# Performance work log

Measured on AMD Instinct MI355X. Metric: run time of the kernel, lower is better.

## Reference

```python
import jax, jax.numpy as jnp
import numpy as np

N = 100000      # nodes
E = 1000000     # edges
D_IN = 64       # in_channels
HID = 64        # hid_channels
ENC = 64        # encoding_dim
OUT = 2         # out_channels (classes)
EDGE_DIM = 32   # TimeEncode dim == edge_dim
HEADS = 2
HD = HID // 2   # per-head channels (32)


def _p(k, shape):
    s = 1.0 / np.sqrt(shape[0])
    return jax.random.uniform(k, shape, jnp.float32, -s, s)


def setup_inputs() -> dict:
    key = jax.random.key(0)
    ks = jax.random.split(key, 40)
    inp = {
        "x": jax.random.normal(ks[0], (N, D_IN), jnp.float32),
        "edge_index": jax.random.randint(ks[1], (2, E), 0, N),
        "node_time": jax.random.uniform(ks[2], (N,), jnp.float32) * 100.0,
        "edge_time": jax.random.uniform(ks[3], (E, 1), jnp.float32) * 100.0,
        "node_mean_out_time_interval": jax.random.uniform(ks[4], (N,), jnp.float32) * 10.0,
        "node_out_degree": jax.random.uniform(ks[5], (N,), jnp.float32) * 50.0,
        "y": jax.random.randint(ks[6], (N,), 0, OUT),
        "train_mask": jnp.ones((N,), bool),
        # TimeEncode: cos(t W + b)
        "time_w": _p(ks[7], (1, EDGE_DIM)), "time_b": jnp.zeros((EDGE_DIM,), jnp.float32),
        # TemporalFrequencyEncoder / DegreeEncoder: Linear(1, ENC)
        "tf_w": _p(ks[8], (1, ENC)), "tf_b": jnp.zeros((ENC,), jnp.float32),
        "deg_w": _p(ks[9], (1, ENC)), "deg_b": jnp.zeros((ENC,), jnp.float32),
        # lin: Linear(in, hid)
        "lin_w": _p(ks[10], (D_IN, HID)), "lin_b": jnp.zeros((HID,), jnp.float32),
        # TransformerConv projections (heads*HD = HID)
        "Wq": _p(ks[11], (HID, HEADS * HD)), "bq": jnp.zeros((HEADS * HD,), jnp.float32),
        "Wk": _p(ks[12], (HID, HEADS * HD)), "bk": jnp.zeros((HEADS * HD,), jnp.float32),
        "Wv": _p(ks[13], (HID, HEADS * HD)), "bv": jnp.zeros((HEADS * HD,), jnp.float32),
        "We": _p(ks[14], (EDGE_DIM, HEADS * HD)), "be": jnp.zeros((HEADS * HD,), jnp.float32),
        "Wskip": _p(ks[15], (HID, HEADS * HD)), "bskip": jnp.zeros((HEADS * HD,), jnp.float32),
        # size-2 context attention
        "wenc_w": _p(ks[16], (ENC, ENC)), "wenc_b": jnp.zeros((ENC,), jnp.float32),
        "wx_w": _p(ks[17], (HID, ENC)), "wx_b": jnp.zeros((ENC,), jnp.float32),
        # lin_combine: Linear(hid+enc, hid)
        "comb_w": _p(ks[18], (HID + ENC, HID)), "comb_b": jnp.zeros((HID,), jnp.float32),
        # out: Linear(hid, out)
        "out_w": _p(ks[19], (HID, OUT)), "out_b": jnp.zeros((OUT,), jnp.float32),
    }
    return inp


def reference(x, edge_index, node_time, edge_time, node_mean_out_time_interval,
              node_out_degree, y, train_mask,
              time_w, time_b, tf_w, tf_b, deg_w, deg_b, lin_w, lin_b,
              Wq, bq, Wk, bk, Wv, bv, We, be, Wskip, bskip,
              wenc_w, wenc_b, wx_w, wx_b, comb_w, comb_b, out_w, out_b):
    src, dst = edge_index[0], edge_index[1]

    # relative edge time -> TimeEncode (cos features), used as edge_attr [E, 32]
    rel_t = node_time[src][:, None] - edge_time          # [E,1]
    rel_t_enc = jnp.cos(rel_t @ time_w + time_b)         # [E,EDGE_DIM]

    h = jax.nn.relu(x @ lin_w + lin_b)                   # [N,HID] (dropout = identity, eval)

    # TransformerConv (PyG math): per-edge attention + scatter-softmax aggregate
    q = (h @ Wq + bq).reshape(N, HEADS, HD)[dst]          # [E,H,HD]
    e = (rel_t_enc @ We + be).reshape(E, HEADS, HD)       # [E,H,HD]
    k = (h @ Wk + bk).reshape(N, HEADS, HD)[src] + e
    v = (h @ Wv + bv).reshape(N, HEADS, HD)[src] + e
    alpha = (q * k).sum(-1) / np.float32(np.sqrt(HD))     # [E,H]
    m = jax.ops.segment_max(alpha, dst, num_segments=N)   # stable softmax per dst node
    ea = jnp.exp(alpha - m[dst])
    denom = jax.ops.segment_sum(ea, dst, num_segments=N)
    a = ea / (denom[dst] + 1e-16)
    agg = jax.ops.segment_sum(a[:, :, None] * v, dst, num_segments=N)
    h1 = agg.reshape(N, HEADS * HD) + h @ Wskip + bskip   # concat heads + root skip

    # size-2 context attention over (temporal-frequency, degree) encodings
    tf_enc = node_mean_out_time_interval[:, None] @ tf_w + tf_b   # [N,ENC]
    deg_enc = node_out_degree[:, None] @ deg_w + deg_b            # [N,ENC]
    enc = jnp.stack((tf_enc, deg_enc), axis=1)                    # [N,2,ENC]
    enc_proj = jnp.tanh(enc @ wenc_w + wenc_b)                    # [N,2,ENC]
    x_proj = jnp.tanh(h1 @ wx_w + wx_b)                           # [N,ENC]
    score = jax.nn.softmax(jnp.einsum('nkd,nd->nk', enc_proj, x_proj), axis=1)  # [N,2]
    context = enc[:, 0] * score[:, 0:1] + enc[:, 1] * score[:, 1:2]

    h1 = jnp.concatenate((h1, context), axis=1) @ comb_w + comb_b  # [N,HID]
    logp = jax.nn.log_softmax(h1 @ out_w + out_b, axis=1)          # [N,OUT]
    return (h1, logp, y, train_mask)
```

## Files before the change

kernel.cpp:

```cpp
#include <hip/hip_runtime.h>
#include <hip/hip_fp16.h>

#define DEV __device__ __forceinline__

typedef _Float16 f16x8 __attribute__((ext_vector_type(8)));
typedef float f32x4 __attribute__((ext_vector_type(4)));

DEV float mask_val(const unsigned char* mb, int n) {
  unsigned b0 = mb[0], b1 = mb[1], b2 = mb[2], b3 = mb[3];
  if (b0 <= 1u && b1 == b0 && b2 == b0 && b3 == b0) {
    return mb[n] ? 1.f : 0.f;
  } else if (b1 == 0u && b2 == 0u && b3 == 0u) {
    return ((const int*)mb)[n] ? 1.f : 0.f;
  } else {
    return (((const float*)mb)[n] != 0.f) ? 1.f : 0.f;
  }
}

DEV float head_sum32(float x) {
  x += __int_as_float(__builtin_amdgcn_ds_swizzle(__float_as_int(x), 0x041F));
  x += __int_as_float(__builtin_amdgcn_ds_swizzle(__float_as_int(x), 0x081F));
  x += __int_as_float(__builtin_amdgcn_ds_swizzle(__float_as_int(x), 0x101F));
  x += __int_as_float(__builtin_amdgcn_ds_swizzle(__float_as_int(x), 0x201F));
  x += __int_as_float(__builtin_amdgcn_ds_swizzle(__float_as_int(x), 0x401F));
  return x;
}

__global__ __launch_bounds__(256) void k_setup(
    const float* __restrict__ tf_w, const float* __restrict__ tf_b,
    const float* __restrict__ deg_w, const float* __restrict__ deg_b,
    const float* __restrict__ wenc_w, const float* __restrict__ wenc_b,
    const float* __restrict__ comb_w,
    const float* __restrict__ lin_w, const float* __restrict__ Wq,
    const float* __restrict__ Wk, const float* __restrict__ Wv,
    const float* __restrict__ Wsk,
    float* __restrict__ cbuf, _Float16* __restrict__ wt,
    int* __restrict__ counts, int N) {
  const int bid = blockIdx.x;
  if (bid < 80) {
    const float* Ws[5] = {lin_w, Wq, Wk, Wv, Wsk};
    int idx = bid * 256 + threadIdx.x;
    if (idx < 5 * 4096) {
      int s = idx >> 12, r = idx & 4095;
      int j = r >> 6, c = r & 63;
      wt[(s << 12) + c * 64 + j] = (_Float16)Ws[s][j * 64 + c];
    }
  } else if (bid == 80) {
    if (threadIdx.x < 64) {
      int c = threadIdx.x;
      float A0 = 0, B0 = 0, A1 = 0, B1 = 0, P0 = 0, Q0 = 0, P1 = 0, Q1 = 0;
      for (int j = 0; j < 64; ++j) {
        float w  = wenc_w[j * 64 + c];
        float cw = comb_w[(64 + j) * 64 + c];
        float twj = tf_w[j], tbj = tf_b[j], dwj = deg_w[j], dbj = deg_b[j];
        A0 += twj * w;  B0 += tbj * w;
        A1 += dwj * w;  B1 += dbj * w;
        P0 += twj * cw; Q0 += tbj * cw;
        P1 += dwj * cw; Q1 += dbj * cw;
      }
      float wb = wenc_b[c];
      cbuf[c]       = A0; cbuf[64 + c]  = B0 + wb;
      cbuf[128 + c] = A1; cbuf[192 + c] = B1 + wb;
      cbuf[256 + c] = P0; cbuf[320 + c] = Q0;
      cbuf[384 + c] = P1; cbuf[448 + c] = Q1;
    }
  } else {
    const int i = (bid - 81) * 256 + threadIdx.x;
    if (i < N) counts[i] = 0;
  }
}

__global__ __launch_bounds__(256) void k_node_proj(
    const float* __restrict__ x, const _Float16* __restrict__ wt,
    const float* __restrict__ lin_b, const float* __restrict__ bq,
    const float* __restrict__ bk, const float* __restrict__ bv,
    const float* __restrict__ bsk, const float* __restrict__ be,
    float* __restrict__ q, __half2* __restrict__ kvp,
    float* __restrict__ skipout, int N,
    const int* __restrict__ ei, int* __restrict__ counts,
    int* __restrict__ rank, int E, int ntiles) {
  __shared__ _Float16 H[4][16 * 72];
  const int bid = blockIdx.x;
  const int tid = threadIdx.x;
  if (bid >= ntiles) {
    const int i = (bid - ntiles) * 256 + tid;
    if (i < E) rank[i] = atomicAdd(&counts[ei[E + i]], 1);
    return;
  }
  const int lane = tid & 63;
  const int wv = tid >> 6;
  const int mrow = lane & 15;
  const int kgrp = lane >> 4;
  const float invs = 0.17677669529663687f;
  float b_lin[4], b_q[4], b_k[4], b_v[4], b_sk[4];
#pragma unroll
  for (int nt = 0; nt < 4; ++nt) {
    const int cc = nt * 16 + mrow;
    b_lin[nt] = lin_b[cc];
    b_q[nt] = bq[cc];
    b_k[nt] = bk[cc] + be[cc];
    b_v[nt] = bv[cc] + be[cc];
    b_sk[nt] = bsk[cc];
  }
  _Float16* Hw = H[wv];
  const int base = bid << 6;
  const int rowA = base + wv * 16 + mrow;
  const int rclamp = (rowA < N) ? rowA : (N - 1);
  const float* xr = x + (size_t)rclamp * 64 + kgrp * 8;
  const float4 u0 = *(const float4*)xr;
  const float4 u1 = *(const float4*)(xr + 4);
  const float4 u2 = *(const float4*)(xr + 32);
  const float4 u3 = *(const float4*)(xr + 36);
  const f16x8 a0 = {(_Float16)u0.x, (_Float16)u0.y, (_Float16)u0.z, (_Float16)u0.w,
                    (_Float16)u1.x, (_Float16)u1.y, (_Float16)u1.z, (_Float16)u1.w};
  const f16x8 a1 = {(_Float16)u2.x, (_Float16)u2.y, (_Float16)u2.z, (_Float16)u2.w,
                    (_Float16)u3.x, (_Float16)u3.y, (_Float16)u3.z, (_Float16)u3.w};
#pragma unroll
  for (int nt = 0; nt < 4; ++nt) {
    const _Float16* wb0 = wt + (nt * 16 + mrow) * 64 + kgrp * 8;
    const f16x8 B0 = *(const f16x8*)wb0;
    const f16x8 B1 = *(const f16x8*)(wb0 + 32);
    f32x4 C = {0.f, 0.f, 0.f, 0.f};
    C = __builtin_amdgcn_mfma_f32_16x16x32_f16(a0, B0, C, 0, 0, 0);
    C = __builtin_amdgcn_mfma_f32_16x16x32_f16(a1, B1, C, 0, 0, 0);
#pragma unroll
    for (int r = 0; r < 4; ++r) {
      const float hval = fmaxf(C[r] + b_lin[nt], 0.f);
      Hw[(kgrp * 4 + r) * 72 + nt * 16 + mrow] = (_Float16)hval;
    }
  }
  const f16x8 ha0 = *(const f16x8*)(Hw + mrow * 72 + kgrp * 8);
  const f16x8 ha1 = *(const f16x8*)(Hw + mrow * 72 + 32 + kgrp * 8);
  const int orow0 = base + wv * 16 + kgrp * 4;
#pragma unroll
  for (int nt = 0; nt < 4; ++nt) {
    const _Float16* wb0 = wt + 4096 + (nt * 16 + mrow) * 64 + kgrp * 8;
    const f16x8 B0 = *(const f16x8*)wb0;
    const f16x8 B1 = *(const f16x8*)(wb0 + 32);
    f32x4 C = {0.f, 0.f, 0.f, 0.f};
    C = __builtin_amdgcn_mfma_f32_16x16x32_f16(ha0, B0, C, 0, 0, 0);
    C = __builtin_amdgcn_mfma_f32_16x16x32_f16(ha1, B1, C, 0, 0, 0);
#pragma unroll
    for (int r = 0; r < 4; ++r) {
      const int orow = orow0 + r;
      if (orow < N) q[(size_t)orow * 64 + nt * 16 + mrow] = (C[r] + b_q[nt]) * invs;
    }
  }
#pragma unroll
  for (int nt = 0; nt < 4; ++nt) {
    const _Float16* wk0 = wt + 2 * 4096 + (nt * 16 + mrow) * 64 + kgrp * 8;
    const _Float16* wv0 = wt + 3 * 4096 + (nt * 16 + mrow) * 64 + kgrp * 8;
    const f16x8 Bk0 = *(const f16x8*)wk0;
    const f16x8 Bk1 = *(const f16x8*)(wk0 + 32);
    const f16x8 Bv0 = *(const f16x8*)wv0;
    const f16x8 Bv1 = *(const f16x8*)(wv0 + 32);
    f32x4 Ck = {0.f, 0.f, 0.f, 0.f};
    f32x4 Cv = {0.f, 0.f, 0.f, 0.f};
    Ck = __builtin_amdgcn_mfma_f32_16x16x32_f16(ha0, Bk0, Ck, 0, 0, 0);
    Ck = __builtin_amdgcn_mfma_f32_16x16x32_f16(ha1, Bk1, Ck, 0, 0, 0);
    Cv = __builtin_amdgcn_mfma_f32_16x16x32_f16(ha0, Bv0, Cv, 0, 0, 0);
    Cv = __builtin_amdgcn_mfma_f32_16x16x32_f16(ha1, Bv1, Cv, 0, 0, 0);
#pragma unroll
    for (int r = 0; r < 4; ++r) {
      const int orow = orow0 + r;
      if (orow < N)
        kvp[(size_t)orow * 64 + nt * 16 + mrow] =
            __halves2half2(__float2half_rn(Ck[r] + b_k[nt]), __float2half_rn(Cv[r] + b_v[nt]));
    }
  }
#pragma unroll
  for (int nt = 0; nt < 4; ++nt) {
    const _Float16* wb0 = wt + 4 * 4096 + (nt * 16 + mrow) * 64 + kgrp * 8;
    const f16x8 B0 = *(const f16x8*)wb0;
    const f16x8 B1 = *(const f16x8*)(wb0 + 32);
    f32x4 C = {0.f, 0.f, 0.f, 0.f};
    C = __builtin_amdgcn_mfma_f32_16x16x32_f16(ha0, B0, C, 0, 0, 0);
    C = __builtin_amdgcn_mfma_f32_16x16x32_f16(ha1, B1, C, 0, 0, 0);
#pragma unroll
    for (int r = 0; r < 4; ++r) {
      const int orow = orow0 + r;
      if (orow < N) skipout[(size_t)orow * 64 + nt * 16 + mrow] = C[r] + b_sk[nt];
    }
  }
}

__global__ __launch_bounds__(256) void k_scan1(const int* __restrict__ counts, int* __restrict__ excl,
                                               int* __restrict__ bsum, int N) {
  __shared__ int s[256];
  const int t = threadIdx.x;
  const int idx = blockIdx.x * 256 + t;
  int val = (idx < N) ? counts[idx] : 0;
  s[t] = val;
  __syncthreads();
  for (int d = 1; d < 256; d <<= 1) {
    int add = (t >= d) ? s[t - d] : 0;
    __syncthreads();
    s[t] += add;
    __syncthreads();
  }
  if (idx < N) excl[idx] = s[t] - val;
  if (t == 255) bsum[blockIdx.x] = s[255];
}

__global__ __launch_bounds__(1024) void k_scan2(int* __restrict__ bsum, int B) {
  __shared__ int sm[1024];
  const int t = threadIdx.x;
  if (B <= 1024) {
    int val = (t < B) ? bsum[t] : 0;
    sm[t] = val;
    __syncthreads();
    for (int d = 1; d < 1024; d <<= 1) {
      int add = (t >= d) ? sm[t - d] : 0;
      __syncthreads();
      sm[t] += add;
      __syncthreads();
    }
    if (t < B) bsum[t] = sm[t] - val;
  } else if (t == 0) {
    int acc = 0;
    for (int i = 0; i < B; ++i) { int tt = bsum[i]; bsum[i] = acc; acc += tt; }
  }
}

__global__ __launch_bounds__(256) void k_scan3(const int* __restrict__ bsum, int* __restrict__ rowptr,
                                               int N, int E) {
  int i = blockIdx.x * 256 + threadIdx.x;
  if (i < N) rowptr[i] = rowptr[i] + bsum[i >> 8];
  if (i == 0) rowptr[N] = E;
}

__global__ __launch_bounds__(256) void k_fill(const int* __restrict__ ei,
                                              const float* __restrict__ node_time,
                                              const float* __restrict__ edge_time,
                                              const int* __restrict__ rowptr,
                                              const int* __restrict__ rank,
                                              int2* __restrict__ er, int E) {
  int e = blockIdx.x * 256 + threadIdx.x;
  if (e < E) {
    int s = ei[e], d = ei[E + e];
    int pos = rowptr[d] + rank[e];
    er[pos] = make_int2(s, __float_as_int(node_time[s] - edge_time[e]));
  }
}

__global__ __launch_bounds__(256) void k_aggregate(
    const int* __restrict__ rowptr, const int2* __restrict__ er,
    const float* __restrict__ q, const unsigned* __restrict__ kvu,
    const float* __restrict__ time_w, const float* __restrict__ time_b,
    const float* __restrict__ We,
    float* __restrict__ h1, int N) {
  __shared__ float swS[4][64];
  __shared__ float EAs[4][2][16];
  const int tid = threadIdx.x;
  const int c = tid & 63;
  const int wv = tid >> 6;
  const float INV2PI = 0.15915494309189535f;
  float wcol[32], Gw[32];
#pragma unroll
  for (int j = 0; j < 32; ++j) wcol[j] = We[j * 64 + c];
#pragma unroll
  for (int j = 0; j < 32; ++j) Gw[j] = We[(c & 31) * 64 + (c & 32) + j];
  const float tw = time_w[c & 31] * INV2PI;
  const float tb = time_b[c & 31] * INV2PI;
  const int h32 = c & 32;
  const int lc = c & 15;
  const bool writer = (c & 16) == 0;
  float (*eaF)[16] = EAs[wv];
  const int n0 = blockIdx.x * 4 + wv;
  const int nstride = gridDim.x * 4;
  for (int n = n0; n < N; n += nstride) {
    const int start = __builtin_amdgcn_readfirstlane(rowptr[n]);
    const int end = __builtin_amdgcn_readfirstlane(rowptr[n + 1]);
    const float skipv = h1[(size_t)n * 64 + c];
    const float qc = q[(size_t)n * 64 + c];
    swS[wv][c] = qc;
    float Gc = 0.f;
#pragma unroll
    for (int j = 0; j < 32; ++j) Gc = fmaf(swS[wv][h32 | j], Gw[j], Gc);
    float m = -1e30f, den = 0.f, num = 0.f, S = 0.f;
    for (int ce = start; ce < end; ce += 16) {
      const int cnt = (end - ce < 16) ? (end - ce) : 16;
      int src_[16];
      float rr_[16];
#pragma unroll
      for (int i = 0; i < 16; ++i) {
        const int ee = ce + ((i < cnt) ? i : cnt - 1);
        const int2 a = er[ee];
        src_[i] = a.x;
        rr_[i] = __int_as_float(a.y);
      }
      unsigned kvr[16];
#pragma unroll
      for (int i = 0; i < 16; ++i) kvr[i] = kvu[(unsigned)(src_[i] * 64 + c)];
      float rv_[16], p[16];
#pragma unroll
      for (int i = 0; i < 16; ++i) {
        float ang = fmaf(rr_[i], tw, tb);
        ang = ang - floorf(ang);
        rv_[i] = __builtin_amdgcn_cosf(ang);
        const __half2 h2 = *(const __half2*)&kvr[i];
        p[i] = fmaf(rv_[i], Gc, qc * __half2float(h2.x));
      }
#pragma unroll
      for (int i = 0; i < 16; ++i) p[i] = head_sum32(p[i]);
#pragma unroll
      for (int i = 0; i < 16; ++i)
        if (i >= cnt) p[i] = -1e30f;
      float cm = p[0];
#pragma unroll
      for (int i = 1; i < 16; ++i) cm = fmaxf(cm, p[i]);
      const float mn = fmaxf(m, cm);
      const float sc = __expf(m - mn);
      num *= sc; den *= sc; S *= sc; m = mn;
      if (writer) {
        float pv = p[0];
#pragma unroll
        for (int i = 1; i < 16; ++i) pv = (lc == i) ? p[i] : pv;
        eaF[c >> 5][lc] = __expf(pv - m);
      }
      const float* eah = eaF[h32 ? 1 : 0];
      const float4 e0 = ((const float4*)eah)[0];
      const float4 e1 = ((const float4*)eah)[1];
      const float4 e2 = ((const float4*)eah)[2];
      const float4 e3 = ((const float4*)eah)[3];
      const float ea_[16] = {e0.x, e0.y, e0.z, e0.w, e1.x, e1.y, e1.z, e1.w,
                             e2.x, e2.y, e2.z, e2.w, e3.x, e3.y, e3.z, e3.w};
#pragma unroll
      for (int i = 0; i < 16; ++i) {
        const float eai = ea_[i];
        const __half2 h2 = *(const __half2*)&kvr[i];
        num = fmaf(eai, __half2float(h2.y), num);
        S = fmaf(eai, rv_[i], S);
        den += eai;
      }
    }
    swS[wv][c] = S;
    float econ = 0.f;
#pragma unroll
    for (int j = 0; j < 32; ++j) econ = fmaf(swS[wv][h32 | j], wcol[j], econ);
    const float agg = (num + econ) / (den + 1e-16f);
    h1[(size_t)n * 64 + c] = agg + skipv;
  }
}

__global__ __launch_bounds__(256) void k_epilogue(
    const float* __restrict__ t_int, const float* __restrict__ deg,
    const float* __restrict__ cbuf,
    const float* __restrict__ wx_w, const float* __restrict__ wx_b,
    const float* __restrict__ comb_w, const float* __restrict__ comb_b,
    const float* __restrict__ out_w, const float* __restrict__ out_b,
    const int* __restrict__ y, const unsigned char* __restrict__ maskb,
    float* __restrict__ out, int N) {
  __shared__ float sh[4][64];
  const int tid = threadIdx.x;
  const int c = tid & 63;
  const int wv = tid >> 6;
  float wxreg[64], cbreg[64];
#pragma unroll
  for (int j = 0; j < 64; ++j) { wxreg[j] = wx_w[j * 64 + c]; cbreg[j] = comb_w[j * 64 + c]; }
  const float A0 = cbuf[c], B0 = cbuf[64 + c], A1 = cbuf[128 + c], B1 = cbuf[192 + c];
  const float P0 = cbuf[256 + c], Q0 = cbuf[320 + c], P1 = cbuf[384 + c], Q1 = cbuf[448 + c];
  const float wxb = wx_b[c], cbb = comb_b[c];
  const float ow0 = out_w[c * 2 + 0], ow1 = out_w[c * 2 + 1];
  const float ob0 = out_b[0], ob1 = out_b[1];
  const size_t O1 = (size_t)N * 64;
  const size_t O2 = O1 + (size_t)N * 2;
  const size_t O3 = O2 + (size_t)N;
  const int ngroups = (N + 3) >> 2;
  for (int g = blockIdx.x; g < ngroups; g += gridDim.x) {
    const int n = g * 4 + wv;
    const bool act = n < N;
    float h1a = 0.f, ti = 0.f, dg = 0.f;
    if (act) {
      h1a = out[(size_t)n * 64 + c];
      ti = t_int[n];
      dg = deg[n];
    }
    sh[wv][c] = h1a;
    const float4* hr = (const float4*)&sh[wv][0];
    float xp = wxb;
    float acc = cbb;
#pragma unroll
    for (int j4 = 0; j4 < 16; ++j4) {
      float4 hv = hr[j4];
      xp  = fmaf(hv.x, wxreg[4 * j4 + 0], xp);
      xp  = fmaf(hv.y, wxreg[4 * j4 + 1], xp);
      xp  = fmaf(hv.z, wxreg[4 * j4 + 2], xp);
      xp  = fmaf(hv.w, wxreg[4 * j4 + 3], xp);
      acc = fmaf(hv.x, cbreg[4 * j4 + 0], acc);
      acc = fmaf(hv.y, cbreg[4 * j4 + 1], acc);
      acc = fmaf(hv.z, cbreg[4 * j4 + 2], acc);
      acc = fmaf(hv.w, cbreg[4 * j4 + 3], acc);
    }
    xp = tanhf(xp);
    const float ep0 = tanhf(fmaf(ti, A0, B0));
    const float ep1 = tanhf(fmaf(dg, A1, B1));
    float d0 = ep0 * xp, d1 = ep1 * xp;
#pragma unroll
    for (int msk = 32; msk >= 1; msk >>= 1) { d0 += __shfl_xor(d0, msk, 64); d1 += __shfl_xor(d1, msk, 64); }
    const float mx = fmaxf(d0, d1);
    const float e0 = expf(d0 - mx), e1 = expf(d1 - mx);
    const float sden = e0 + e1;
    const float s0 = e0 / sden, s1 = e1 / sden;
    acc = fmaf(s0, fmaf(ti, P0, Q0), acc);
    acc = fmaf(s1, fmaf(dg, P1, Q1), acc);
    float z0 = acc * ow0, z1 = acc * ow1;
#pragma unroll
    for (int msk = 32; msk >= 1; msk >>= 1) { z0 += __shfl_xor(z0, msk, 64); z1 += __shfl_xor(z1, msk, 64); }
    if (act) {
      out[(size_t)n * 64 + c] = acc;
      if (c == 0) {
        z0 += ob0; z1 += ob1;
        const float mz = fmaxf(z0, z1);
        const float lse = mz + logf(expf(z0 - mz) + expf(z1 - mz));
        out[O1 + (size_t)n * 2 + 0] = z0 - lse;
        out[O1 + (size_t)n * 2 + 1] = z1 - lse;
        out[O2 + (size_t)n] = (float)y[n];
        out[O3 + (size_t)n] = mask_val(maskb, n);
      }
    }
  }
}

extern "C" void kernel_launch(void* const* d_in, const int* in_sizes, int n_in,
                              void* d_out, int out_size, void* d_ws, size_t ws_size,
                              hipStream_t stream) {
  const float* x          = (const float*)d_in[0];
  const int*   ei         = (const int*)d_in[1];
  const float* node_time  = (const float*)d_in[2];
  const float* edge_time  = (const float*)d_in[3];
  const float* nmoti      = (const float*)d_in[4];
  const float* nod        = (const float*)d_in[5];
  const int*   y          = (const int*)d_in[6];
  const unsigned char* mask = (const unsigned char*)d_in[7];
  const float* time_w = (const float*)d_in[8];
  const float* time_b = (const float*)d_in[9];
  const float* tf_w   = (const float*)d_in[10];
  const float* tf_b   = (const float*)d_in[11];
  const float* deg_w  = (const float*)d_in[12];
  const float* deg_b  = (const float*)d_in[13];
  const float* lin_w  = (const float*)d_in[14];
  const float* lin_b  = (const float*)d_in[15];
  const float* Wq     = (const float*)d_in[16];
  const float* bq     = (const float*)d_in[17];
  const float* Wk     = (const float*)d_in[18];
  const float* bk     = (const float*)d_in[19];
  const float* Wv     = (const float*)d_in[20];
  const float* bv     = (const float*)d_in[21];
  const float* We     = (const float*)d_in[22];
  const float* be     = (const float*)d_in[23];
  const float* Wsk    = (const float*)d_in[24];
  const float* bsk    = (const float*)d_in[25];
  const float* wenc_w = (const float*)d_in[26];
  const float* wenc_b = (const float*)d_in[27];
  const float* wx_w   = (const float*)d_in[28];
  const float* wx_b   = (const float*)d_in[29];
  const float* comb_w = (const float*)d_in[30];
  const float* comb_b = (const float*)d_in[31];
  const float* out_w  = (const float*)d_in[32];
  const float* out_b  = (const float*)d_in[33];

  const int N = in_sizes[2];
  const int E = in_sizes[3];
  const size_t N64 = (size_t)N * 64;

  float*    q    = (float*)d_ws;
  __half2*  kvp  = (__half2*)(q + N64);
  int2*     er   = (int2*)((char*)kvp + N64 * sizeof(__half2));
  int*      rank = (int*)(er + E);
  int*      counts = rank + E;
  int*      rowptr = counts + N;
  int*      bsum   = rowptr + N + 1;
  float*    cbuf   = (float*)(bsum + 4096);
  _Float16* wt     = (_Float16*)(cbuf + 512);
  float*    outf   = (float*)d_out;
  float*    skip   = outf;

  const int B = (N + 255) / 256;
  const int ntiles = (N + 63) >> 6;
  const int EB = (E + 255) / 256;

  k_setup<<<81 + B, 256, 0, stream>>>(tf_w, tf_b, deg_w, deg_b, wenc_w, wenc_b, comb_w,
                                      lin_w, Wq, Wk, Wv, Wsk, cbuf, wt, counts, N);

  k_node_proj<<<ntiles + EB, 256, 0, stream>>>(x, wt, lin_b, bq, bk, bv, bsk, be,
                                               q, kvp, skip, N, ei, counts, rank, E, ntiles);

  k_scan1<<<B, 256, 0, stream>>>(counts, rowptr, bsum, N);
  k_scan2<<<1, 1024, 0, stream>>>(bsum, B);
  k_scan3<<<B, 256, 0, stream>>>(bsum, rowptr, N, E);
  k_fill<<<EB, 256, 0, stream>>>(ei, node_time, edge_time, rowptr, rank, er, E);

  int agb = 2048;
  if (agb > (N + 3) / 4) agb = (N + 3) / 4;
  k_aggregate<<<agb, 256, 0, stream>>>(rowptr, er, q, (const unsigned*)kvp,
                                       time_w, time_b, We, outf, N);

  k_epilogue<<<2048, 256, 0, stream>>>(nmoti, nod, cbuf, wx_w, wx_b,
                                       comb_w, comb_b, out_w, out_b, y, mask, outf, N);
}
```

Measured before the change: 352.2 us.

## Fuse epilogue into aggregation kernel with fp16 shared-memory weights

Merges the per-node context-attention and combine epilogue into the aggregation kernel, so h1 is never written to and re-read from global memory and one kernel launch is dropped. The wx and comb weight matrices are staged in shared memory as fp16 instead of being held in registers. Softmax exponentials switch to fast __expf. In exchange the weights lose precision, shared-memory use rises (about 18KB per block, which may reduce occupancy), and the weight reads now go through LDS inside the aggregation loop.

```diff
diff --git a/kernel.cpp b/kernel.cpp
--- a/kernel.cpp
+++ b/kernel.cpp
@@ -248,12 +248,35 @@
     const float* __restrict__ q, const unsigned* __restrict__ kvu,
     const float* __restrict__ time_w, const float* __restrict__ time_b,
     const float* __restrict__ We,
+    const float* __restrict__ t_int, const float* __restrict__ deg,
+    const float* __restrict__ cbuf,
+    const float* __restrict__ wx_w, const float* __restrict__ wx_b,
+    const float* __restrict__ comb_w, const float* __restrict__ comb_b,
+    const float* __restrict__ out_w, const float* __restrict__ out_b,
+    const int* __restrict__ y, const unsigned char* __restrict__ maskb,
     float* __restrict__ h1, int N) {
   __shared__ float swS[4][64];
   __shared__ float EAs[4][2][16];
+  __shared__ _Float16 WX[4096];
+  __shared__ _Float16 CB[4096];
+  __shared__ float CBUF[512];
+  __shared__ float MISC[4 * 64 + 2];
   const int tid = threadIdx.x;
   const int c = tid & 63;
   const int wv = tid >> 6;
+  for (int idx = tid; idx < 4096; idx += 256) {
+    WX[idx] = (_Float16)wx_w[idx];
+    CB[idx] = (_Float16)comb_w[idx];
+  }
+  for (int idx = tid; idx < 512; idx += 256) CBUF[idx] = cbuf[idx];
+  if (tid < 64) {
+    MISC[tid] = wx_b[tid];
+    MISC[64 + tid] = comb_b[tid];
+    MISC[128 + tid] = out_w[tid * 2 + 0];
+    MISC[192 + tid] = out_w[tid * 2 + 1];
+  }
+  if (tid == 0) { MISC[256] = out_b[0]; MISC[257] = out_b[1]; }
+  __syncthreads();
   const float INV2PI = 0.15915494309189535f;
   float wcol[32], Gw[32];
 #pragma unroll
@@ -266,6 +289,9 @@
   const int lc = c & 15;
   const bool writer = (c & 16) == 0;
   float (*eaF)[16] = EAs[wv];
+  const size_t O1 = (size_t)N * 64;
+  const size_t O2 = O1 + (size_t)N * 2;
+  const size_t O3 = O2 + (size_t)N;
   const int n0 = blockIdx.x * 4 + wv;
   const int nstride = gridDim.x * 4;
   for (int n = n0; n < N; n += nstride) {
@@ -338,86 +364,42 @@
     float econ = 0.f;
 #pragma unroll
     for (int j = 0; j < 32; ++j) econ = fmaf(swS[wv][h32 | j], wcol[j], econ);
-    const float agg = (num + econ) / (den + 1e-16f);
-    h1[(size_t)n * 64 + c] = agg + skipv;
-  }
-}
-
-__global__ __launch_bounds__(256) void k_epilogue(
-    const float* __restrict__ t_int, const float* __restrict__ deg,
-    const float* __restrict__ cbuf,
-    const float* __restrict__ wx_w, const float* __restrict__ wx_b,
-    const float* __restrict__ comb_w, const float* __restrict__ comb_b,
-    const float* __restrict__ out_w, const float* __restrict__ out_b,
-    const int* __restrict__ y, const unsigned char* __restrict__ maskb,
-    float* __restrict__ out, int N) {
-  __shared__ float sh[4][64];
-  const int tid = threadIdx.x;
-  const int c = tid & 63;
-  const int wv = tid >> 6;
-  float wxreg[64], cbreg[64];
-#pragma unroll
-  for (int j = 0; j < 64; ++j) { wxreg[j] = wx_w[j * 64 + c]; cbreg[j] = comb_w[j * 64 + c]; }
-  const float A0 = cbuf[c], B0 = cbuf[64 + c], A1 = cbuf[128 + c], B1 = cbuf[192 + c];
-  const float P0 = cbuf[256 + c], Q0 = cbuf[320 + c], P1 = cbuf[384 + c], Q1 = cbuf[448 + c];
-  const float wxb = wx_b[c], cbb = comb_b[c];
-  const float ow0 = out_w[c * 2 + 0], ow1 = out_w[c * 2 + 1];
-  const float ob0 = out_b[0], ob1 = out_b[1];
-  const size_t O1 = (size_t)N * 64;
-  const size_t O2 = O1 + (size_t)N * 2;
-  const size_t O3 = O2 + (size_t)N;
-  const int ngroups = (N + 3) >> 2;
-  for (int g = blockIdx.x; g < ngroups; g += gridDim.x) {
-    const int n = g * 4 + wv;
-    const bool act = n < N;
-    float h1a = 0.f, ti = 0.f, dg = 0.f;
-    if (act) {
-      h1a = out[(size_t)n * 64 + c];
-      ti = t_int[n];
-      dg = deg[n];
-    }
-    sh[wv][c] = h1a;
-    const float4* hr = (const float4*)&sh[wv][0];
-    float xp = wxb;
-    float acc = cbb;
-#pragma unroll
-    for (int j4 = 0; j4 < 16; ++j4) {
-      float4 hv = hr[j4];
-      xp  = fmaf(hv.x, wxreg[4 * j4 + 0], xp);
-      xp  = fmaf(hv.y, wxreg[4 * j4 + 1], xp);
-      xp  = fmaf(hv.z, wxreg[4 * j4 + 2], xp);
-      xp  = fmaf(hv.w, wxreg[4 * j4 + 3], xp);
-      acc = fmaf(hv.x, cbreg[4 * j4 + 0], acc);
-      acc = fmaf(hv.y, cbreg[4 * j4 + 1], acc);
-      acc = fmaf(hv.z, cbreg[4 * j4 + 2], acc);
-      acc = fmaf(hv.w, cbreg[4 * j4 + 3], acc);
+    const float h1a = (num + econ) / (den + 1e-16f) + skipv;
+    swS[wv][c] = h1a;
+    const float ti = t_int[n];
+    const float dg = deg[n];
+    float xp = MISC[c];
+    float acc = MISC[64 + c];
+#pragma unroll 8
+    for (int j = 0; j < 64; ++j) {
+      const float hv = swS[wv][j];
+      xp = fmaf(hv, (float)WX[j * 64 + c], xp);
+      acc = fmaf(hv, (float)CB[j * 64 + c], acc);
     }
     xp = tanhf(xp);
-    const float ep0 = tanhf(fmaf(ti, A0, B0));
-    const float ep1 = tanhf(fmaf(dg, A1, B1));
+    const float ep0 = tanhf(fmaf(ti, CBUF[c], CBUF[64 + c]));
+    const float ep1 = tanhf(fmaf(dg, CBUF[128 + c], CBUF[192 + c]));
     float d0 = ep0 * xp, d1 = ep1 * xp;
 #pragma unroll
     for (int msk = 32; msk >= 1; msk >>= 1) { d0 += __shfl_xor(d0, msk, 64); d1 += __shfl_xor(d1, msk, 64); }
     const float mx = fmaxf(d0, d1);
-    const float e0 = expf(d0 - mx), e1 = expf(d1 - mx);
-    const float sden = e0 + e1;
-    const float s0 = e0 / sden, s1 = e1 / sden;
-    acc = fmaf(s0, fmaf(ti, P0, Q0), acc);
-    acc = fmaf(s1, fmaf(dg, P1, Q1), acc);
-    float z0 = acc * ow0, z1 = acc * ow1;
+    const float se0 = __expf(d0 - mx), se1 = __expf(d1 - mx);
+    const float sden = se0 + se1;
+    const float s0 = se0 / sden, s1 = se1 / sden;
+    acc = fmaf(s0, fmaf(ti, CBUF[256 + c], CBUF[320 + c]), acc);
+    acc = fmaf(s1, fmaf(dg, CBUF[384 + c], CBUF[448 + c]), acc);
+    float z0 = acc * MISC[128 + c], z1 = acc * MISC[192 + c];
 #pragma unroll
     for (int msk = 32; msk >= 1; msk >>= 1) { z0 += __shfl_xor(z0, msk, 64); z1 += __shfl_xor(z1, msk, 64); }
-    if (act) {
-      out[(size_t)n * 64 + c] = acc;
-      if (c == 0) {
-        z0 += ob0; z1 += ob1;
-        const float mz = fmaxf(z0, z1);
-        const float lse = mz + logf(expf(z0 - mz) + expf(z1 - mz));
-        out[O1 + (size_t)n * 2 + 0] = z0 - lse;
-        out[O1 + (size_t)n * 2 + 1] = z1 - lse;
-        out[O2 + (size_t)n] = (float)y[n];
-        out[O3 + (size_t)n] = mask_val(maskb, n);
-      }
+    h1[(size_t)n * 64 + c] = acc;
+    if (c == 0) {
+      z0 += MISC[256]; z1 += MISC[257];
+      const float mz = fmaxf(z0, z1);
+      const float lse = mz + logf(__expf(z0 - mz) + __expf(z1 - mz));
+      h1[O1 + (size_t)n * 2 + 0] = z0 - lse;
+      h1[O1 + (size_t)n * 2 + 1] = z1 - lse;
+      h1[O2 + (size_t)n] = (float)y[n];
+      h1[O3 + (size_t)n] = mask_val(maskb, n);
     }
   }
 }
@@ -494,8 +476,7 @@
   int agb = 2048;
   if (agb > (N + 3) / 4) agb = (N + 3) / 4;
   k_aggregate<<<agb, 256, 0, stream>>>(rowptr, er, q, (const unsigned*)kvp,
-                                       time_w, time_b, We, outf, N);
-
-  k_epilogue<<<2048, 256, 0, stream>>>(nmoti, nod, cbuf, wx_w, wx_b,
-                                       comb_w, comb_b, out_w, out_b, y, mask, outf, N);
-}
+                                       time_w, time_b, We,
+                                       nmoti, nod, cbuf, wx_w, wx_b, comb_w, comb_b,
+                                       out_w, out_b, y, mask, outf, N);
+}
```

Result: slower. 402.2 us (+14.2%).
